# Kernel optimization log

Measured on AMD Instinct MI355X. Metric: run time of the kernel, lower is better.

The kernel has to match this reference:

```python
import jax, jax.numpy as jnp
import numpy as np

B, S, D, H = 4, 2048, 1024, 16
HD = D // H


def setup_inputs() -> dict:
    key = jax.random.key(0)
    ks = jax.random.split(key, 11)
    s = 1.0 / np.sqrt(D)
    inp = {
        "query": jax.random.normal(ks[0], (B, S, D), jnp.float32),
        "key": jax.random.normal(ks[1], (B, S, D), jnp.float32),
        "value": jax.random.normal(ks[2], (B, S, D), jnp.float32),
        "Wq": jax.random.normal(ks[3], (D, D), jnp.float32) * s,
        "bq": jnp.zeros((D,), jnp.float32),
        "Wk": jax.random.normal(ks[4], (D, D), jnp.float32) * s,
        "bk": jnp.zeros((D,), jnp.float32),
        "Wv": jax.random.normal(ks[5], (D, D), jnp.float32) * s,
        "bv": jnp.zeros((D,), jnp.float32),
        "Wo": jax.random.normal(ks[6], (D, D), jnp.float32) * s,
        "bo": jnp.zeros((D,), jnp.float32),
    }
    return inp


def reference(query, key, value, Wq, bq, Wk, bk, Wv, bv, Wo, bo):
    scale = 1.0 / np.sqrt(HD).astype(np.float32)
    # Linear projections (torch Linear: x @ W.T + b), split into heads -> [B,H,S,HD]
    def proj(x, W, b):
        y = x @ W.T + b
        return y.reshape(B, S, H, HD).transpose(0, 2, 1, 3)

    q = proj(query, Wq, bq)
    k = proj(key, Wk, bk)
    v = proj(value, Wv, bv)
    scores = jnp.einsum("bhqd,bhkd->bhqk", q, k) * scale  # [B,H,S,S]
    weights = jax.nn.softmax(scores, axis=-1)
    attn = jnp.einsum("bhqk,bhkd->bhqd", weights, v)
    attn = attn.transpose(0, 2, 1, 3).reshape(B, S, D)
    return attn @ Wo.T + bo
```

## Files before the change

### kernel.cpp

```cpp
#include <hip/hip_runtime.h>
#include <hip/hip_bf16.h>
#include <stdint.h>

#define Bn 4
#define Sn 2048
#define Dn 1024
#define Hn 16
#define HDn 64
#define Mn (Bn * Sn)
#define PS 44

typedef __attribute__((ext_vector_type(8))) __bf16 bf16x8;
typedef __attribute__((ext_vector_type(4))) __bf16 bf16x4;
typedef __attribute__((ext_vector_type(4))) float f32x4;

#if __has_builtin(__builtin_amdgcn_exp2f)
#define EXP2F(x) __builtin_amdgcn_exp2f(x)
#else
#define EXP2F(x) exp2f(x)
#endif

typedef __attribute__((address_space(1))) unsigned int as1_uint;
typedef __attribute__((address_space(3))) unsigned int as3_uint;

__device__ __forceinline__ void gld_lds16(const void* g, void* l) {
  __builtin_amdgcn_global_load_lds((const as1_uint*)g, (as3_uint*)l, 16, 0, 0);
}

struct CvtArgs {
  const float* src[7];
};
__constant__ const size_t kGb[8] = {0,       1048576, 2097152, 3145728,
                                    3276800, 3407872, 3538944, 3670016};

__global__ __launch_bounds__(256) void cvt_all(CvtArgs a, __bf16* __restrict__ dst) {
  size_t i = (size_t)blockIdx.x * 256 + threadIdx.x;
  if (i >= 3670016) return;
  int s = 0;
#pragma unroll
  for (int k = 1; k < 7; k++) s += (i >= kGb[k]) ? 1 : 0;
  const float4* sp = (const float4*)a.src[s] + 2 * (i - kGb[s]);
  float4 x = sp[0], y = sp[1];
  bf16x8 o;
  o[0] = (__bf16)x.x; o[1] = (__bf16)x.y; o[2] = (__bf16)x.z; o[3] = (__bf16)x.w;
  o[4] = (__bf16)y.x; o[5] = (__bf16)y.y; o[6] = (__bf16)y.z; o[7] = (__bf16)y.w;
  *(bf16x8*)(dst + 8 * i) = o;
}

template <int MODE>
__device__ __forceinline__ void gemm128_body(const __bf16* __restrict__ A,
                                             const __bf16* __restrict__ Bw,
                                             const float* __restrict__ bias,
                                             void* __restrict__ Cout, int m0, int n0,
                                             float scale) {
  __shared__ __align__(16) __bf16 lA[128 * 32];
  __shared__ __align__(16) __bf16 lB[128 * 32];
  const int tid = threadIdx.x;
  const int wave = tid >> 6, lane = tid & 63, quad = lane >> 4, l15 = lane & 15;
  const int wm = wave >> 1, wn = wave & 1;
  f32x4 acc[4][4] = {};
  const char* Ab = (const char*)(A + (size_t)m0 * Dn);
  const char* Bb = (const char*)(Bw + (size_t)n0 * Dn);
  char* lAc = (char*)lA;
  char* lBc = (char*)lB;
  const int o0 = tid * 16, o1 = o0 + 4096;
  const int r0 = o0 >> 6, c0 = o0 & 63;
  const int r1 = o1 >> 6, c1 = o1 & 63;

  for (int k0 = 0; k0 < Dn; k0 += 32) {
    __syncthreads();
    gld_lds16(Ab + (size_t)r0 * 2048 + k0 * 2 + c0, lAc + o0);
    gld_lds16(Ab + (size_t)r1 * 2048 + k0 * 2 + c1, lAc + o1);
    gld_lds16(Bb + (size_t)r0 * 2048 + k0 * 2 + c0, lBc + o0);
    gld_lds16(Bb + (size_t)r1 * 2048 + k0 * 2 + c1, lBc + o1);
    __syncthreads();
    bf16x8 af[4], bfv[4];
#pragma unroll
    for (int i = 0; i < 4; i++)
      af[i] = *(const bf16x8*)(lA + (wm * 64 + i * 16 + l15) * 32 + quad * 8);
#pragma unroll
    for (int t = 0; t < 4; t++)
      bfv[t] = *(const bf16x8*)(lB + (wn * 64 + t * 16 + l15) * 32 + quad * 8);
#pragma unroll
    for (int i = 0; i < 4; i++)
#pragma unroll
      for (int t = 0; t < 4; t++)
        acc[i][t] = __builtin_amdgcn_mfma_f32_16x16x32_bf16(af[i], bfv[t], acc[i][t], 0, 0, 0);
  }
#pragma unroll
  for (int i = 0; i < 4; i++) {
    const int rowb = m0 + wm * 64 + i * 16 + quad * 4;
#pragma unroll
    for (int t = 0; t < 4; t++) {
      const int col = n0 + wn * 64 + t * 16 + l15;
      const float bb = bias[col];
      if (MODE == 2) {
        const int b = rowb >> 11, s = rowb & 2047;
        const int h = col >> 6, c = col & 63;
        bf16x4 pk;
#pragma unroll
        for (int r = 0; r < 4; r++) pk[r] = (__bf16)(acc[i][t][r] + bb);
        *(bf16x4*)((__bf16*)Cout + (((size_t)(b * Hn + h) * HDn + c) * Sn + s)) = pk;
      } else {
#pragma unroll
        for (int r = 0; r < 4; r++) {
          float v = (acc[i][t][r] + bb) * scale;
          if (MODE == 1)
            ((float*)Cout)[(size_t)(rowb + r) * Dn + col] = v;
          else
            ((__bf16*)Cout)[(size_t)(rowb + r) * Dn + col] = (__bf16)v;
        }
      }
    }
  }
}

__global__ __launch_bounds__(256, 3) void qkv_gemm(
    const __bf16* __restrict__ X, const __bf16* __restrict__ W,
    const float* __restrict__ bq, const float* __restrict__ bk,
    const float* __restrict__ bv, __bf16* __restrict__ out) {
  const int z = blockIdx.z;
  const int m0 = blockIdx.y * 128, n0 = blockIdx.x * 128;
  if (z == 0) {
    gemm128_body<0>(X, W, bq, out, m0, n0, 0.18033688011112042f);
  } else if (z == 1) {
    gemm128_body<0>(X + (size_t)Mn * Dn, W + (size_t)Dn * Dn, bk,
                    out + (size_t)Mn * Dn, m0, n0, 1.0f);
  } else {
    gemm128_body<2>(X + 2 * (size_t)Mn * Dn, W + 2 * (size_t)Dn * Dn, bv,
                    out + 2 * (size_t)Mn * Dn, m0, n0, 1.0f);
  }
}

__global__ __launch_bounds__(256, 3) void out_gemm(const __bf16* __restrict__ A,
                                                   const __bf16* __restrict__ W,
                                                   const float* __restrict__ bo,
                                                   float* __restrict__ out) {
  gemm128_body<1>(A, W, bo, out, blockIdx.y * 128, blockIdx.x * 128, 1.0f);
}

__global__ __launch_bounds__(256, 2) void flash_attn(const __bf16* __restrict__ Q,
                                                     const __bf16* __restrict__ K,
                                                     const __bf16* __restrict__ Vt,
                                                     __bf16* __restrict__ Aout) {
  __shared__ __align__(16) __bf16 plds[4][64 * PS];
  __shared__ __align__(16) float om[2][4][64 * 4];
  __shared__ float lim[2][4][64];
  const int tid = threadIdx.x;
  const int wave = tid >> 6, lane = tid & 63, quad = lane >> 4, l15 = lane & 15;
  const int qw = wave & 1, half = wave >> 1;
  const int lin = blockIdx.x + (blockIdx.y << 4);
  const int wg = (lin & 7) * 128 + (lin >> 3);
  const int bh = wg >> 4, qt = wg & 15;
  const int b = bh >> 4, h = bh & 15;
  const int q0 = qt * 128 + qw * 64;
  const int k0base = half * (Sn / 2);
  const __bf16* Qb = Q + ((size_t)b * Sn) * Dn + h * HDn;
  const __bf16* Kb = K + ((size_t)b * Sn) * Dn + h * HDn;
  const __bf16* Vtb = Vt + (size_t)(b * Hn + h) * HDn * Sn;
  __bf16* myP = &plds[wave][0];

  bf16x8 qf[4][2];
#pragma unroll
  for (int iq = 0; iq < 4; iq++)
#pragma unroll
    for (int s = 0; s < 2; s++)
      qf[iq][s] = *(const bf16x8*)(Qb + (size_t)(q0 + iq * 16 + l15) * Dn + s * 32 + quad * 8);

  f32x4 O[4][4] = {};
  float li[4] = {};

  bf16x8 kf[2][2][2];
  bf16x8 vf[2][4];
#pragma unroll
  for (int tk = 0; tk < 2; tk++)
#pragma unroll
    for (int s = 0; s < 2; s++)
      kf[0][tk][s] =
          *(const bf16x8*)(Kb + (size_t)(k0base + tk * 16 + l15) * Dn + s * 32 + quad * 8);
#pragma unroll
  for (int mc = 0; mc < 4; mc++)
    vf[0][mc] = *(const bf16x8*)(Vtb + (size_t)(mc * 16 + l15) * Sn + k0base + quad * 8);

#pragma unroll 2
  for (int kt = 0; kt < Sn / 64; kt++) {
    const int cur = kt & 1, nxt = cur ^ 1;
    f32x4 sa[2][4];
#pragma unroll
    for (int tk = 0; tk < 2; tk++)
#pragma unroll
      for (int iq = 0; iq < 4; iq++) {
        f32x4 z = {0.f, 0.f, 0.f, 0.f};
        z = __builtin_amdgcn_mfma_f32_16x16x32_bf16(kf[cur][tk][0], qf[iq][0], z, 0, 0, 0);
        z = __builtin_amdgcn_mfma_f32_16x16x32_bf16(kf[cur][tk][1], qf[iq][1], z, 0, 0, 0);
        sa[tk][iq] = z;
      }
    if (kt < Sn / 64 - 1) {
      const int key0 = k0base + (kt + 1) * 32;
#pragma unroll
      for (int tk = 0; tk < 2; tk++)
#pragma unroll
        for (int s = 0; s < 2; s++)
          kf[nxt][tk][s] =
              *(const bf16x8*)(Kb + (size_t)(key0 + tk * 16 + l15) * Dn + s * 32 + quad * 8);
#pragma unroll
      for (int mc = 0; mc < 4; mc++)
        vf[nxt][mc] = *(const bf16x8*)(Vtb + (size_t)(mc * 16 + l15) * Sn + key0 + quad * 8);
    }
#pragma unroll
    for (int tk = 0; tk < 2; tk++)
#pragma unroll
      for (int iq = 0; iq < 4; iq++) {
        bf16x4 pk;
#pragma unroll
        for (int r = 0; r < 4; r++) {
          float p = EXP2F(sa[tk][iq][r]);
          li[iq] += p;
          pk[r] = (__bf16)p;
        }
        *(bf16x4*)(myP + (iq * 16 + l15) * PS + tk * 16 + quad * 4) = pk;
      }
#pragma unroll
    for (int iq = 0; iq < 4; iq++) {
      bf16x4 plo = *(const bf16x4*)(myP + (iq * 16 + l15) * PS + quad * 8);
      bf16x4 phi = *(const bf16x4*)(myP + (iq * 16 + l15) * PS + quad * 8 + 4);
      bf16x8 pf = __builtin_shufflevector(plo, phi, 0, 1, 2, 3, 4, 5, 6, 7);
#pragma unroll
      for (int mc = 0; mc < 4; mc++)
        O[mc][iq] = __builtin_amdgcn_mfma_f32_16x16x32_bf16(vf[cur][mc], pf, O[mc][iq], 0, 0, 0);
    }
  }

#pragma unroll
  for (int mc = 0; mc < 4; mc++) {
    __syncthreads();
    if (half) {
#pragma unroll
      for (int iq = 0; iq < 4; iq++) *(f32x4*)&om[qw][iq][lane * 4] = O[mc][iq];
      if (mc == 0)
#pragma unroll
        for (int iq = 0; iq < 4; iq++) lim[qw][iq][lane] = li[iq];
    }
    __syncthreads();
    if (!half) {
#pragma unroll
      for (int iq = 0; iq < 4; iq++) O[mc][iq] += *(const f32x4*)&om[qw][iq][lane * 4];
      if (mc == 0)
#pragma unroll
        for (int iq = 0; iq < 4; iq++) li[iq] += lim[qw][iq][lane];
    }
  }
  if (half) return;

  float inv[4];
#pragma unroll
  for (int iq = 0; iq < 4; iq++) {
    float s = li[iq];
    s += __shfl_xor(s, 16);
    s += __shfl_xor(s, 32);
    inv[iq] = 1.0f / s;
  }
#pragma unroll
  for (int mc = 0; mc < 4; mc++)
#pragma unroll
    for (int iq = 0; iq < 4; iq++) {
      bf16x4 o;
#pragma unroll
      for (int r = 0; r < 4; r++) o[r] = (__bf16)(O[mc][iq][r] * inv[iq]);
      *(bf16x4*)(Aout + ((size_t)b * Sn + q0 + iq * 16 + l15) * Dn + h * HDn + mc * 16 +
                 quad * 4) = o;
    }
}

extern "C" void kernel_launch(void* const* d_in, const int* in_sizes, int n_in,
                              void* d_out, int out_size, void* d_ws, size_t ws_size,
                              hipStream_t stream) {
  const float* bq = (const float*)d_in[4];
  const float* bk = (const float*)d_in[6];
  const float* bv = (const float*)d_in[8];
  const float* bo = (const float*)d_in[10];

  const size_t MD = (size_t)Mn * Dn;
  const size_t DD = (size_t)Dn * Dn;
  __bf16* Xbf  = (__bf16*)d_ws;
  __bf16* Wbf  = Xbf + 3 * MD;
  __bf16* QKV  = Wbf + 4 * DD;
  __bf16* Attn = QKV + 3 * MD;

  CvtArgs ca;
  ca.src[0] = (const float*)d_in[0];
  ca.src[1] = (const float*)d_in[1];
  ca.src[2] = (const float*)d_in[2];
  ca.src[3] = (const float*)d_in[3];
  ca.src[4] = (const float*)d_in[5];
  ca.src[5] = (const float*)d_in[7];
  ca.src[6] = (const float*)d_in[9];
  cvt_all<<<14336, 256, 0, stream>>>(ca, Xbf);

  qkv_gemm<<<dim3(Dn / 128, Mn / 128, 3), 256, 0, stream>>>(Xbf, Wbf, bq, bk, bv, QKV);
  flash_attn<<<dim3(Sn / 128, Bn * Hn), 256, 0, stream>>>(QKV, QKV + MD, QKV + 2 * MD, Attn);
  out_gemm<<<dim3(Dn / 128, Mn / 128), 256, 0, stream>>>(Attn, Wbf + 3 * DD, bo, (float*)d_out);
}
```

Measured before the change: 392.5 us.

## Software-pipeline QK^T MFMA of next tile with softmax and PV of current

Restructures the attention inner loop so the QK^T MFMAs for key tile kt+1 are issued before the exp/softmax and PV MFMAs of tile kt. Two score buffers alternate and the loop is manually unrolled by two. K and V are prefetched two tiles ahead into double-buffered registers, with the prefetch index clamped at the end. This is meant to hide MFMA latency and the exp/LDS round-trip behind independent matrix work. The cost is extra score registers, which may lower occupancy, plus one redundant QK^T computation on the final step.

```diff
diff --git a/kernel.cpp b/kernel.cpp
--- a/kernel.cpp
+++ b/kernel.cpp
@@ -9,6 +9,7 @@
 #define HDn 64
 #define Mn (Bn * Sn)
 #define PS 44
+#define NT (Sn / 64)
 
 typedef __attribute__((ext_vector_type(8))) __bf16 bf16x8;
 typedef __attribute__((ext_vector_type(4))) __bf16 bf16x4;
@@ -172,64 +173,73 @@
 
   bf16x8 kf[2][2][2];
   bf16x8 vf[2][4];
+  f32x4 saA[2][4], saB[2][4];
+
 #pragma unroll
   for (int tk = 0; tk < 2; tk++)
 #pragma unroll
-    for (int s = 0; s < 2; s++)
+    for (int s = 0; s < 2; s++) {
       kf[0][tk][s] =
           *(const bf16x8*)(Kb + (size_t)(k0base + tk * 16 + l15) * Dn + s * 32 + quad * 8);
-#pragma unroll
-  for (int mc = 0; mc < 4; mc++)
+      kf[1][tk][s] =
+          *(const bf16x8*)(Kb + (size_t)(k0base + 32 + tk * 16 + l15) * Dn + s * 32 + quad * 8);
+    }
+#pragma unroll
+  for (int mc = 0; mc < 4; mc++) {
     vf[0][mc] = *(const bf16x8*)(Vtb + (size_t)(mc * 16 + l15) * Sn + k0base + quad * 8);
-
-#pragma unroll 2
-  for (int kt = 0; kt < Sn / 64; kt++) {
-    const int cur = kt & 1, nxt = cur ^ 1;
-    f32x4 sa[2][4];
-#pragma unroll
-    for (int tk = 0; tk < 2; tk++)
-#pragma unroll
-      for (int iq = 0; iq < 4; iq++) {
-        f32x4 z = {0.f, 0.f, 0.f, 0.f};
-        z = __builtin_amdgcn_mfma_f32_16x16x32_bf16(kf[cur][tk][0], qf[iq][0], z, 0, 0, 0);
-        z = __builtin_amdgcn_mfma_f32_16x16x32_bf16(kf[cur][tk][1], qf[iq][1], z, 0, 0, 0);
-        sa[tk][iq] = z;
-      }
-    if (kt < Sn / 64 - 1) {
-      const int key0 = k0base + (kt + 1) * 32;
-#pragma unroll
-      for (int tk = 0; tk < 2; tk++)
-#pragma unroll
-        for (int s = 0; s < 2; s++)
-          kf[nxt][tk][s] =
-              *(const bf16x8*)(Kb + (size_t)(key0 + tk * 16 + l15) * Dn + s * 32 + quad * 8);
-#pragma unroll
-      for (int mc = 0; mc < 4; mc++)
-        vf[nxt][mc] = *(const bf16x8*)(Vtb + (size_t)(mc * 16 + l15) * Sn + key0 + quad * 8);
-    }
-#pragma unroll
-    for (int tk = 0; tk < 2; tk++)
-#pragma unroll
-      for (int iq = 0; iq < 4; iq++) {
-        bf16x4 pk;
-#pragma unroll
-        for (int r = 0; r < 4; r++) {
-          float p = EXP2F(sa[tk][iq][r]);
-          li[iq] += p;
-          pk[r] = (__bf16)p;
-        }
-        *(bf16x4*)(myP + (iq * 16 + l15) * PS + tk * 16 + quad * 4) = pk;
-      }
+    vf[1][mc] = *(const bf16x8*)(Vtb + (size_t)(mc * 16 + l15) * Sn + k0base + 32 + quad * 8);
+  }
+#pragma unroll
+  for (int tk = 0; tk < 2; tk++)
 #pragma unroll
     for (int iq = 0; iq < 4; iq++) {
-      bf16x4 plo = *(const bf16x4*)(myP + (iq * 16 + l15) * PS + quad * 8);
-      bf16x4 phi = *(const bf16x4*)(myP + (iq * 16 + l15) * PS + quad * 8 + 4);
-      bf16x8 pf = __builtin_shufflevector(plo, phi, 0, 1, 2, 3, 4, 5, 6, 7);
-#pragma unroll
-      for (int mc = 0; mc < 4; mc++)
-        O[mc][iq] = __builtin_amdgcn_mfma_f32_16x16x32_bf16(vf[cur][mc], pf, O[mc][iq], 0, 0, 0);
-    }
-  }
+      f32x4 z = {0.f, 0.f, 0.f, 0.f};
+      z = __builtin_amdgcn_mfma_f32_16x16x32_bf16(kf[0][tk][0], qf[iq][0], z, 0, 0, 0);
+      z = __builtin_amdgcn_mfma_f32_16x16x32_bf16(kf[0][tk][1], qf[iq][1], z, 0, 0, 0);
+      saA[tk][iq] = z;
+    }
+
+#define MFMA16(a_, b_, c_) __builtin_amdgcn_mfma_f32_16x16x32_bf16(a_, b_, c_, 0, 0, 0)
+#define KSTEP(KT, CUR, NXT, SA_C, SA_N)                                                  \
+  {                                                                                      \
+    _Pragma("unroll") for (int tk = 0; tk < 2; tk++)                                     \
+        _Pragma("unroll") for (int iq = 0; iq < 4; iq++) {                               \
+      f32x4 z = {0.f, 0.f, 0.f, 0.f};                                                    \
+      z = MFMA16(kf[NXT][tk][0], qf[iq][0], z);                                          \
+      z = MFMA16(kf[NXT][tk][1], qf[iq][1], z);                                          \
+      SA_N[tk][iq] = z;                                                                  \
+    }                                                                                    \
+    const int keyn = k0base + ((((KT) + 2) < NT) ? ((KT) + 2) : (NT - 1)) * 32;          \
+    _Pragma("unroll") for (int tk = 0; tk < 2; tk++)                                     \
+        _Pragma("unroll") for (int s = 0; s < 2; s++) kf[CUR][tk][s] =                   \
+            *(const bf16x8*)(Kb + (size_t)(keyn + tk * 16 + l15) * Dn + s * 32 + quad * 8); \
+    _Pragma("unroll") for (int tk = 0; tk < 2; tk++)                                     \
+        _Pragma("unroll") for (int iq = 0; iq < 4; iq++) {                               \
+      bf16x4 pk;                                                                         \
+      _Pragma("unroll") for (int r = 0; r < 4; r++) {                                    \
+        float p = EXP2F(SA_C[tk][iq][r]);                                                \
+        li[iq] += p;                                                                     \
+        pk[r] = (__bf16)p;                                                               \
+      }                                                                                  \
+      *(bf16x4*)(myP + (iq * 16 + l15) * PS + tk * 16 + quad * 4) = pk;                  \
+    }                                                                                    \
+    _Pragma("unroll") for (int iq = 0; iq < 4; iq++) {                                   \
+      bf16x4 plo = *(const bf16x4*)(myP + (iq * 16 + l15) * PS + quad * 8);              \
+      bf16x4 phi = *(const bf16x4*)(myP + (iq * 16 + l15) * PS + quad * 8 + 4);          \
+      bf16x8 pf = __builtin_shufflevector(plo, phi, 0, 1, 2, 3, 4, 5, 6, 7);             \
+      _Pragma("unroll") for (int mc = 0; mc < 4; mc++)                                   \
+          O[mc][iq] = MFMA16(vf[CUR][mc], pf, O[mc][iq]);                                \
+    }                                                                                    \
+    _Pragma("unroll") for (int mc = 0; mc < 4; mc++) vf[CUR][mc] =                       \
+        *(const bf16x8*)(Vtb + (size_t)(mc * 16 + l15) * Sn + keyn + quad * 8);          \
+  }
+
+  for (int kt = 0; kt < NT; kt += 2) {
+    KSTEP(kt, 0, 1, saA, saB)
+    KSTEP(kt + 1, 1, 0, saB, saA)
+  }
+#undef KSTEP
+#undef MFMA16
 
 #pragma unroll
   for (int mc = 0; mc < 4; mc++) {
```

Measured after the change: 412.5 us. 5.1% more time.
